# Kernel optimization log

Measured on AMD Instinct MI355X. Metric: run time of the kernel, lower is better.

## Reference

```python
import jax, jax.numpy as jnp
import numpy as np

NUM_SLOTS = 7
DIM = 4096
NUM_HEADS = 8
HEAD_DIM = DIM // NUM_HEADS
LN_EPS = 1e-5


def setup_inputs() -> dict:
    key = jax.random.key(0)
    ks = jax.random.split(key, 9)
    B, N = 8, 2048
    x = jax.random.normal(ks[0], (B, N, DIM), dtype=jnp.float32)
    slots = 1e-4 * jax.random.normal(ks[1], (NUM_SLOTS, DIM), dtype=jnp.float32)
    ln_g = jnp.ones((DIM,), jnp.float32)
    ln_b = jnp.zeros((DIM,), jnp.float32)
    # nn.MultiheadAttention packed in-projection: rows [Wq; Wk; Wv], each (DIM, DIM)
    s = 1.0 / np.sqrt(DIM)
    in_proj_w = jax.random.uniform(ks[2], (3 * DIM, DIM), jnp.float32, -s, s)
    in_proj_b = jnp.zeros((3 * DIM,), jnp.float32)
    out_proj_w = jax.random.uniform(ks[3], (DIM, DIM), jnp.float32, -s, s)
    out_proj_b = jnp.zeros((DIM,), jnp.float32)
    alpha = 0.1 * jax.random.normal(ks[4], (1,), jnp.float32)  # nonzero so gate path is active
    return {"x": x, "slots": slots, "ln_g": ln_g, "ln_b": ln_b,
            "in_proj_w": in_proj_w, "in_proj_b": in_proj_b,
            "out_proj_w": out_proj_w, "out_proj_b": out_proj_b, "alpha": alpha}


def _cmrm(x, slots, ln_g, ln_b, in_proj_w, in_proj_b, out_proj_w, out_proj_b, alpha):
    x32 = x.astype(jnp.float32)
    # pre LayerNorm
    mu = jnp.mean(x32, axis=-1, keepdims=True)
    var = jnp.mean(jnp.square(x32 - mu), axis=-1, keepdims=True)
    xn = (x32 - mu) * jax.lax.rsqrt(var + LN_EPS) * ln_g + ln_b  # (B,N,D)
    slots_c = jnp.clip(slots, -10.0, 10.0)  # (Q,D), Q=7
    Wq, Wk, Wv = jnp.split(in_proj_w, 3, axis=0)
    bq, bk, bv = jnp.split(in_proj_b, 3, axis=0)
    q = slots_c @ Wq.T + bq                      # (Q,D), identical for all batches
    k = xn @ Wk.T + bk                           # (B,N,D)
    v = xn @ Wv.T + bv                           # (B,N,D)
    B, N, _ = x.shape
    qh = q.reshape(NUM_SLOTS, NUM_HEADS, HEAD_DIM)          # (Q,H,hd)
    kh = k.reshape(B, N, NUM_HEADS, HEAD_DIM)
    vh = v.reshape(B, N, NUM_HEADS, HEAD_DIM)
    scale = 1.0 / np.sqrt(HEAD_DIM)
    scores = jnp.einsum('qhd,bnhd->bhqn', qh * scale, kh)   # (B,H,Q,N)
    attn = jax.nn.softmax(scores, axis=-1)
    ctx = jnp.einsum('bhqn,bnhd->bqhd', attn, vh).reshape(B, NUM_SLOTS, DIM)
    slots_out = ctx @ out_proj_w.T + out_proj_b             # (B,Q,D)
    slots_res = slots_c[None] + slots_out                   # residual, ungated slots
    gate = jnp.tanh(alpha)                                  # (1,)
    g = jnp.mean(gate * slots_res, axis=1, keepdims=True)   # (B,1,D)
    x_refined = (x32 + g).astype(x.dtype)
    attn_weights = jnp.mean(attn, axis=1)                   # torch avg over heads -> (B,Q,N)
    return x_refined, attn_weights


def reference(x, slots, ln_g, ln_b, in_proj_w, in_proj_b, out_proj_w, out_proj_b, alpha):
    return _cmrm(x, slots, ln_g, ln_b, in_proj_w, in_proj_b, out_proj_w, out_proj_b, alpha)
```

## Files before the change

kernel.cpp:

```cpp
#include <hip/hip_runtime.h>

typedef __attribute__((ext_vector_type(4))) float f32x4;
typedef __attribute__((ext_vector_type(8))) short short8x;
typedef __attribute__((ext_vector_type(4))) unsigned short u16x4;

#define DIM   4096
#define NB    8
#define NN    2048
#define NROWS (NB*NN)
#define NQ    7
#define NHQ   56
#define SCALE 0.04419417382415922f

#define OFF_MU     0L
#define OFF_RSTD   16384L
#define OFF_Q7     32768L
#define OFF_A      61440L
#define OFF_D0     61504L
#define OFF_S1     61568L
#define OFF_SUMEXP 61632L
#define OFF_CTXM   62528L
#define OFF_GFIN   95296L
#define OFF_YM     128064L
#define OFF_UGBF   390208L
#define OFF_SCT    521280L
#define OFF_BIG    1438784L
#define OFF_PART   (OFF_BIG)
#define OFF_XBF    10000000L

__device__ __forceinline__ unsigned short f2bf(float f) {
  union { float f; unsigned int u; } v; v.f = f;
  return (unsigned short)((v.u + 0x7FFFu + ((v.u >> 16) & 1u)) >> 16);
}
__device__ __forceinline__ unsigned short f2bfr(float f) {
  union { float f; unsigned int u; } v; v.f = f;
  return (unsigned short)((v.u + 0x8000u) >> 16);
}
__device__ __forceinline__ float bf2f(unsigned short u) {
  return __uint_as_float((unsigned)u << 16);
}
__device__ __forceinline__ f32x4 ntl4(const float* p) {
  return __builtin_nontemporal_load((const f32x4*)p);
}
__device__ __forceinline__ void nts4(float* p, f32x4 v) {
  __builtin_nontemporal_store(v, (f32x4*)p);
}
__device__ __forceinline__ float waveSum(float v) {
  #pragma unroll
  for (int m = 1; m < 64; m <<= 1) v += __shfl_xor(v, m);
  return v;
}

__global__ __launch_bounds__(256) void k_pre(const float* __restrict__ ipw,
    const float* __restrict__ ipb, const float* __restrict__ slots,
    float* __restrict__ q7, float* __restrict__ ws) {
  const int bid = blockIdx.x, tid = threadIdx.x;
  const int w = tid >> 6, l = tid & 63;
  if (bid == 0) {
    if (tid < 448) (ws + OFF_SUMEXP)[tid] = 0.f;
    else if (tid < 512) (ws + OFF_S1)[tid - 448] = 0.f;
  } else if (bid <= 8) {
    unsigned* u32 = (unsigned*)(ws + OFF_UGBF);
    const long r = 56 + bid - 1;
    #pragma unroll
    for (int j = 0; j < 8; j++) u32[r*2048 + (long)tid*8 + j] = 0u;
  } else if (bid == 9) {
    if (tid < 64) (ws + OFF_A)[tid] = 0.f;
    else if (tid < 128) (ws + OFF_D0)[tid - 64] = 0.f;
  }
  const int d = bid * 4 + w;
  const float* wr = ipw + (long)d * DIM;
  float acc[7] = {0,0,0,0,0,0,0};
  for (int e4 = l; e4 < 1024; e4 += 64) {
    f32x4 wv = ntl4(wr + e4*4);
    #pragma unroll
    for (int s = 0; s < 7; s++) {
      float4 sv = ((const float4*)(slots + (long)s*DIM))[e4];
      sv.x = fminf(fmaxf(sv.x, -10.f), 10.f); sv.y = fminf(fmaxf(sv.y, -10.f), 10.f);
      sv.z = fminf(fmaxf(sv.z, -10.f), 10.f); sv.w = fminf(fmaxf(sv.w, -10.f), 10.f);
      acc[s] += wv.x*sv.x + wv.y*sv.y + wv.z*sv.z + wv.w*sv.w;
    }
  }
  #pragma unroll
  for (int s = 0; s < 7; s++) acc[s] = waveSum(acc[s]);
  if (l == 0) {
    float bq = ipb[d];
    #pragma unroll
    for (int s = 0; s < 7; s++) q7[(long)s*DIM + d] = acc[s] + bq;
  }
}

__global__ __launch_bounds__(256) void k_uproj(const float* __restrict__ ipw,
    const float* __restrict__ ipb, const float* __restrict__ q7,
    float* __restrict__ upart, float* __restrict__ D0arr) {
  __shared__ float qs[7][32];
  const int bid = blockIdx.x, tid = threadIdx.x;
  const int bx = bid & 3, h = (bid >> 2) & 7, c = bid >> 5;
  if (tid < 224) {
    int s = tid >> 5, hd = tid & 31;
    qs[s][hd] = q7[(long)s*DIM + h*512 + c*32 + hd];
  }
  __syncthreads();
  if (bx == 0 && tid < 64) {
    const int l = tid;
    float bk = (l < 32) ? ipb[DIM + h*512 + c*32 + l] : 0.f;
    #pragma unroll
    for (int s = 0; s < 7; s++) {
      float v = (l < 32) ? qs[s][l]*bk : 0.f;
      v = waveSum(v);
      if (l == 0) atomicAdd(&D0arr[h*7 + s], SCALE * v);
    }
  }
  const int e0 = bx*1024 + tid*4;
  float4 acc[7];
  #pragma unroll
  for (int s = 0; s < 7; s++) { acc[s].x = 0; acc[s].y = 0; acc[s].z = 0; acc[s].w = 0; }
  #pragma unroll 4
  for (int hd = 0; hd < 32; hd++) {
    f32x4 wv = ntl4(ipw + ((long)(DIM + h*512 + c*32 + hd))*DIM + e0);
    #pragma unroll
    for (int s = 0; s < 7; s++) {
      float qv = qs[s][hd];
      acc[s].x += qv*wv.x; acc[s].y += qv*wv.y; acc[s].z += qv*wv.z; acc[s].w += qv*wv.w;
    }
  }
  #pragma unroll
  for (int s = 0; s < 7; s++)
    *(float4*)&upart[(long)((c*8 + h)*7 + s)*DIM + e0] = acc[s];
}

__global__ __launch_bounds__(256) void k_ured(const float* __restrict__ upart,
    const float* __restrict__ lng, const float* __restrict__ lnb,
    unsigned short* __restrict__ ugbf, float* __restrict__ Aarr, float* __restrict__ D0arr) {
  const int bid = blockIdx.x, tid = threadIdx.x;
  const int bx = bid & 15, h = bid >> 4;
  const int e = bx*256 + tid, l = tid & 63;
  float ge = lng[e], be = lnb[e];
  #pragma unroll
  for (int s = 0; s < 7; s++) {
    float u = 0;
    #pragma unroll
    for (int c = 0; c < 16; c++) u += upart[(long)((c*8 + h)*7 + s)*DIM + e];
    u *= SCALE;
    ugbf[(long)(h*7 + s)*DIM + e] = f2bf(u * ge);
    float pa = waveSum(u * ge);
    float pd = waveSum(u * be);
    if (l == 0) {
      atomicAdd(&Aarr[h*7 + s], pa);
      atomicAdd(&D0arr[h*7 + s], pd);
    }
  }
}

__global__ __launch_bounds__(256) void k_scores(const float* __restrict__ x,
    const unsigned short* __restrict__ ugbf, const float* __restrict__ Aarr,
    const float* __restrict__ D0arr, float* __restrict__ mu_o, float* __restrict__ rstd_o,
    float* __restrict__ sct, float* __restrict__ sumexp, unsigned short* __restrict__ xbf) {
  __shared__ __align__(16) unsigned short xs[16][520];
  __shared__ float xch[3][64][16];
  __shared__ float sred[16][2];
  const int tid = threadIdx.x;
  const int w = tid >> 6, l = tid & 63;
  const int lr = l & 15, lk8 = (l >> 4) * 8;
  const int row0 = blockIdx.x * 16;
  const int b = blockIdx.x >> 7;
  const int r = tid >> 4, c = tid & 15;
  const long xrow = (long)(row0 + r) * DIM;
  f32x4 acc0 = {0,0,0,0}, acc1 = {0,0,0,0}, acc2 = {0,0,0,0}, acc3 = {0,0,0,0};
  float sx = 0.f, sxx = 0.f;
  const long b0 = (long)(0*16 + lr)*DIM, b1 = (long)(1*16 + lr)*DIM,
             b2 = (long)(2*16 + lr)*DIM, b3 = (long)(3*16 + lr)*DIM;
  for (int s = 0; s < 8; s++) {
    const int kc0 = s * 512;
    f32x4 v[8];
    #pragma unroll
    for (int j = 0; j < 8; j++)
      v[j] = ntl4(x + xrow + kc0 + j*64 + c*4);
    #pragma unroll
    for (int j = 0; j < 8; j++) {
      sx  += (v[j].x + v[j].y) + (v[j].z + v[j].w);
      sxx += v[j].x*v[j].x + v[j].y*v[j].y + v[j].z*v[j].z + v[j].w*v[j].w;
      u16x4 a;
      a.x = f2bfr(v[j].x); a.y = f2bfr(v[j].y);
      a.z = f2bfr(v[j].z); a.w = f2bfr(v[j].w);
      *(u16x4*)&xs[r][j*64 + c*4] = a;
      *(u16x4*)(xbf + xrow + kc0 + j*64 + c*4) = a;
    }
    __syncthreads();
    const long kw = kc0 + w*128;
    #pragma unroll
    for (int kk = 0; kk < 128; kk += 32) {
      short8x a = *(const short8x*)&xs[lr][w*128 + kk + lk8];
      short8x bb0 = *(const short8x*)(ugbf + b0 + kw + kk + lk8);
      acc0 = __builtin_amdgcn_mfma_f32_16x16x32_bf16(a, bb0, acc0, 0, 0, 0);
      short8x bb1 = *(const short8x*)(ugbf + b1 + kw + kk + lk8);
      acc1 = __builtin_amdgcn_mfma_f32_16x16x32_bf16(a, bb1, acc1, 0, 0, 0);
      short8x bb2 = *(const short8x*)(ugbf + b2 + kw + kk + lk8);
      acc2 = __builtin_amdgcn_mfma_f32_16x16x32_bf16(a, bb2, acc2, 0, 0, 0);
      short8x bb3 = *(const short8x*)(ugbf + b3 + kw + kk + lk8);
      acc3 = __builtin_amdgcn_mfma_f32_16x16x32_bf16(a, bb3, acc3, 0, 0, 0);
    }
    __syncthreads();
  }
  #pragma unroll
  for (int m = 1; m <= 8; m <<= 1) { sx += __shfl_xor(sx, m); sxx += __shfl_xor(sxx, m); }
  if (c == 0) { sred[r][0] = sx; sred[r][1] = sxx; }
  if (w != 0) {
    float* p = xch[w - 1][l];
    #pragma unroll
    for (int i = 0; i < 4; i++) {
      p[i] = acc0[i]; p[4+i] = acc1[i]; p[8+i] = acc2[i]; p[12+i] = acc3[i];
    }
  }
  __syncthreads();
  if (w != 0) return;
  #pragma unroll
  for (int ww = 0; ww < 3; ww++) {
    const float* p = xch[ww][l];
    #pragma unroll
    for (int i = 0; i < 4; i++) {
      acc0[i] += p[i]; acc1[i] += p[4+i]; acc2[i] += p[8+i]; acc3[i] += p[12+i];
    }
  }
  float muv = sred[lr][0] * (1.0f/DIM);
  float var = sred[lr][1] * (1.0f/DIM) - muv*muv;
  float rsv = rsqrtf(var + 1e-5f);
  if (l < 16) { mu_o[row0 + l] = muv; rstd_o[row0 + l] = rsv; }
  float es0 = 0, es1 = 0, es2 = 0, es3 = 0;
  #pragma unroll
  for (int i = 0; i < 4; i++) {
    const int rl = (l >> 4)*4 + i;
    const float mur_ = __shfl(muv, rl);
    const float rs_  = __shfl(rsv, rl);
    {
      int hq = 0*16 + lr; float Ah = Aarr[hq], Dh = D0arr[hq];
      float e = __expf(rs_*(acc0[i] - mur_*Ah) + Dh);
      sct[(long)hq*NROWS + row0 + rl] = e; es0 += e;
    }
    {
      int hq = 1*16 + lr; float Ah = Aarr[hq], Dh = D0arr[hq];
      float e = __expf(rs_*(acc1[i] - mur_*Ah) + Dh);
      sct[(long)hq*NROWS + row0 + rl] = e; es1 += e;
    }
    {
      int hq = 2*16 + lr; float Ah = Aarr[hq], Dh = D0arr[hq];
      float e = __expf(rs_*(acc2[i] - mur_*Ah) + Dh);
      sct[(long)hq*NROWS + row0 + rl] = e; es2 += e;
    }
    if (lr < 8) {
      int hq = 3*16 + lr; float Ah = Aarr[hq], Dh = D0arr[hq];
      float e = __expf(rs_*(acc3[i] - mur_*Ah) + Dh);
      sct[(long)hq*NROWS + row0 + rl] = e; es3 += e;
    }
  }
  es0 += __shfl_xor(es0, 16); es0 += __shfl_xor(es0, 32);
  es1 += __shfl_xor(es1, 16); es1 += __shfl_xor(es1, 32);
  es2 += __shfl_xor(es2, 16); es2 += __shfl_xor(es2, 32);
  es3 += __shfl_xor(es3, 16); es3 += __shfl_xor(es3, 32);
  if (l < 16) {
    atomicAdd(&sumexp[b*NHQ + 0*16 + l], es0);
    atomicAdd(&sumexp[b*NHQ + 1*16 + l], es1);
    atomicAdd(&sumexp[b*NHQ + 2*16 + l], es2);
    if (l < 8) atomicAdd(&sumexp[b*NHQ + 3*16 + l], es3);
  }
}

__global__ __launch_bounds__(256) void k_ypart(const unsigned short* __restrict__ xbf,
    const float* __restrict__ sct, const float* __restrict__ sumexp,
    const float* __restrict__ mu, const float* __restrict__ rstd,
    float* __restrict__ part, float* __restrict__ s1, float* __restrict__ out_attn) {
  __shared__ float rinv[56];
  __shared__ float amr[8][128];
  __shared__ float psm[56][128];
  const int bid = blockIdx.x, tid = threadIdx.x;
  const int b = bid >> 6, ec = (bid >> 4) & 3, nc = bid & 15;
  const int row0 = b*NN + nc*128;
  if (tid < 56) rinv[tid] = 1.0f / sumexp[b*NHQ + tid];
  __syncthreads();
  for (int i = tid; i < 1024; i += 256) {
    const int h = i >> 7, nn = i & 127, row = row0 + nn;
    float amv = 0;
    #pragma unroll
    for (int q = 0; q < 7; q++) {
      float p = sct[(long)(h*7 + q)*NROWS + row] * rinv[h*7 + q];
      amv += p;
      psm[h*7 + q][nn] = p;
    }
    amv *= (1.0f/7.0f);
    amr[h][nn] = amv * rstd[row];
  }
  __syncthreads();
  if (ec == 0) {
    for (int i = tid; i < 896; i += 256) {
      const int q = i / 128, nn = i % 128;
      float s = 0;
      #pragma unroll
      for (int h = 0; h < 8; h++) s += psm[h*7 + q][nn];
      out_attn[((long)(b*NQ + q))*NN + nc*128 + nn] = s * 0.125f;
    }
    {
      const int h = tid >> 5, sl = tid & 31;
      float v = 0;
      #pragma unroll
      for (int nn = sl; nn < 128; nn += 32) v += amr[h][nn] * mu[row0 + nn];
      #pragma unroll
      for (int m = 1; m < 32; m <<= 1) v += __shfl_xor(v, m);
      if (sl == 0) atomicAdd(&s1[b*8 + h], v);
    }
  }
  const int e = ec*1024 + tid*4;
  float ax[8], ay[8], az[8], aw[8];
  #pragma unroll
  for (int h = 0; h < 8; h++) { ax[h]=0; ay[h]=0; az[h]=0; aw[h]=0; }
  const unsigned short* xp = xbf + (long)row0*DIM + e;
  #pragma unroll 2
  for (int nn = 0; nn < 128; nn++) {
    const u16x4 xv = *(const u16x4*)(xp + (long)nn*DIM);
    const float xx = bf2f(xv.x), xy = bf2f(xv.y), xz = bf2f(xv.z), xw = bf2f(xv.w);
    #pragma unroll
    for (int h = 0; h < 8; h++) {
      float a = amr[h][nn];
      ax[h] += a*xx; ay[h] += a*xy; az[h] += a*xz; aw[h] += a*xw;
    }
  }
  #pragma unroll
  for (int h = 0; h < 8; h++) {
    float4 o; o.x = ax[h]; o.y = ay[h]; o.z = az[h]; o.w = aw[h];
    *(float4*)&part[((long)(nc*64 + b*8 + h))*DIM + e] = o;
  }
}

__global__ __launch_bounds__(256) void k_yred(const float* __restrict__ part,
    const float* __restrict__ s1, const float* __restrict__ lng, const float* __restrict__ lnb,
    float* __restrict__ ym) {
  const long i4 = (long)blockIdx.x*256 + threadIdx.x;
  const float4* p4 = (const float4*)part;
  float4 s = p4[i4];
  #pragma unroll
  for (int nc = 1; nc < 16; nc++) {
    float4 v = p4[(long)nc*65536 + i4];
    s.x += v.x; s.y += v.y; s.z += v.z; s.w += v.w;
  }
  const int bh = (int)(i4 >> 10), e4 = (int)(i4 & 1023);
  float sv = s1[bh];
  float4 g = ((const float4*)lng)[e4], bb = ((const float4*)lnb)[e4];
  float4 o;
  o.x = g.x*(s.x - sv) + bb.x; o.y = g.y*(s.y - sv) + bb.y;
  o.z = g.z*(s.z - sv) + bb.z; o.w = g.w*(s.w - sv) + bb.w;
  ((float4*)ym)[i4] = o;
}

__global__ __launch_bounds__(256) void k_ctxm(const float* __restrict__ ipw,
    const float* __restrict__ ipb, const float* __restrict__ ym, float* __restrict__ ctxm) {
  const int w = threadIdx.x >> 6, l = threadIdx.x & 63;
  const int d = blockIdx.x*4 + w;
  const int h = d >> 9;
  const float* wr = ipw + ((long)(2*DIM + d))*DIM;
  float acc[8] = {0,0,0,0,0,0,0,0};
  for (int e4 = l; e4 < 1024; e4 += 64) {
    f32x4 wv = ntl4(wr + e4*4);
    #pragma unroll
    for (int b = 0; b < 8; b++) {
      float4 y = ((const float4*)(ym + (long)(b*8 + h)*DIM))[e4];
      acc[b] += wv.x*y.x + wv.y*y.y + wv.z*y.z + wv.w*y.w;
    }
  }
  #pragma unroll
  for (int b = 0; b < 8; b++) acc[b] = waveSum(acc[b]);
  if (l == 0) {
    float bias = ipb[2*DIM + d];
    #pragma unroll
    for (int b = 0; b < 8; b++) ctxm[(long)b*DIM + d] = acc[b] + bias;
  }
}

__global__ __launch_bounds__(256) void k_gvec(const float* __restrict__ opw,
    const float* __restrict__ opb, const float* __restrict__ ctxm, const float* __restrict__ slots,
    const float* __restrict__ alpha, float* __restrict__ gfin) {
  const int w = threadIdx.x >> 6, l = threadIdx.x & 63;
  const int d = blockIdx.x*4 + w;
  const float* wr = opw + (long)d*DIM;
  float acc[8] = {0,0,0,0,0,0,0,0};
  for (int e4 = l; e4 < 1024; e4 += 64) {
    f32x4 wv = ntl4(wr + e4*4);
    #pragma unroll
    for (int b = 0; b < 8; b++) {
      float4 c = ((const float4*)(ctxm + (long)b*DIM))[e4];
      acc[b] += wv.x*c.x + wv.y*c.y + wv.z*c.z + wv.w*c.w;
    }
  }
  #pragma unroll
  for (int b = 0; b < 8; b++) acc[b] = waveSum(acc[b]);
  if (l == 0) {
    float smv = 0;
    #pragma unroll
    for (int q = 0; q < 7; q++)
      smv += fminf(fmaxf(slots[(long)q*DIM + d], -10.f), 10.f);
    smv *= (1.0f/7.0f);
    float t = tanhf(alpha[0]);
    float base = smv + opb[d];
    #pragma unroll
    for (int b = 0; b < 8; b++) gfin[(long)b*DIM + d] = t * (base + acc[b]);
  }
}

__global__ __launch_bounds__(256) void k_refine(const unsigned short* __restrict__ xbf,
    const float* __restrict__ gfin, float* __restrict__ out) {
  const float4* g4 = (const float4*)gfin;
  const long total = (long)NROWS * 1024;
  for (long i4 = (long)blockIdx.x*256 + threadIdx.x; i4 < total; i4 += (long)gridDim.x*256) {
    const long b = i4 >> 21;
    const int e4 = (int)(i4 & 1023);
    const u16x4 xv = *(const u16x4*)(xbf + i4*4);
    const float4 gv = g4[b*1024 + e4];
    f32x4 o;
    o.x = bf2f(xv.x) + gv.x; o.y = bf2f(xv.y) + gv.y;
    o.z = bf2f(xv.z) + gv.z; o.w = bf2f(xv.w) + gv.w;
    nts4(out + i4*4, o);
  }
}

extern "C" void kernel_launch(void* const* d_in, const int* in_sizes, int n_in,
                              void* d_out, int out_size, void* d_ws, size_t ws_size,
                              hipStream_t stream) {
  const float* x     = (const float*)d_in[0];
  const float* slots = (const float*)d_in[1];
  const float* lng   = (const float*)d_in[2];
  const float* lnb   = (const float*)d_in[3];
  const float* ipw   = (const float*)d_in[4];
  const float* ipb   = (const float*)d_in[5];
  const float* opw   = (const float*)d_in[6];
  const float* opb   = (const float*)d_in[7];
  const float* alpha = (const float*)d_in[8];
  float* out = (float*)d_out;
  float* ws  = (float*)d_ws;

  float* mu     = ws + OFF_MU;
  float* rstd   = ws + OFF_RSTD;
  float* q7     = ws + OFF_Q7;
  float* Aarr   = ws + OFF_A;
  float* D0arr  = ws + OFF_D0;
  float* s1     = ws + OFF_S1;
  float* sumexp = ws + OFF_SUMEXP;
  float* ctxm   = ws + OFF_CTXM;
  float* gfin   = ws + OFF_GFIN;
  float* ym     = ws + OFF_YM;
  unsigned short* ugbf = (unsigned short*)(ws + OFF_UGBF);
  float* sct    = ws + OFF_SCT;
  float* upart  = ws + OFF_BIG;
  float* part   = ws + OFF_PART;
  unsigned short* xbf = (unsigned short*)(ws + OFF_XBF);
  float* out_attn = out + (long)NROWS * DIM;

  hipLaunchKernelGGL(k_pre,    dim3(1024), dim3(256), 0, stream, ipw, ipb, slots, q7, ws);
  hipLaunchKernelGGL(k_uproj,  dim3(512),  dim3(256), 0, stream, ipw, ipb, q7, upart, D0arr);
  hipLaunchKernelGGL(k_ured,   dim3(128),  dim3(256), 0, stream, upart, lng, lnb, ugbf, Aarr, D0arr);
  hipLaunchKernelGGL(k_scores, dim3(1024), dim3(256), 0, stream, x, ugbf, Aarr, D0arr, mu, rstd, sct, sumexp, xbf);
  hipLaunchKernelGGL(k_ypart,  dim3(512),  dim3(256), 0, stream, xbf, sct, sumexp, mu, rstd, part, s1, out_attn);
  hipLaunchKernelGGL(k_yred,   dim3(256),  dim3(256), 0, stream, part, s1, lng, lnb, ym);
  hipLaunchKernelGGL(k_ctxm,   dim3(1024), dim3(256), 0, stream, ipw, ipb, ym, ctxm);
  hipLaunchKernelGGL(k_gvec,   dim3(1024), dim3(256), 0, stream, opw, opb, ctxm, slots, alpha, gfin);
  hipLaunchKernelGGL(k_refine, dim3(8192), dim3(256), 0, stream, xbf, gfin, out);
}
```

Baseline: 348.1 us.

## Double-buffer x tiles in k_scores to overlap global loads with MFMA

The k_scores loop now uses two LDS buffers and prefetches the next 512-column chunk of x into registers while the current chunk's MFMAs run. It then converts the prefetched data to bf16 and writes it to the other buffer. This halves the barriers per iteration and hides global load latency behind compute. Each thread also handles 8 contiguous elements (16-byte bf16 stores) instead of 4, widening the LDS and xbf stores. The cost is doubled LDS for xs and higher register pressure from the prefetch registers, which could reduce occupancy.

New measurement: 388.1 us. +11.5%, slower.

```diff
diff --git a/kernel.cpp b/kernel.cpp
--- a/kernel.cpp
+++ b/kernel.cpp
@@ -156,7 +156,7 @@
     const unsigned short* __restrict__ ugbf, const float* __restrict__ Aarr,
     const float* __restrict__ D0arr, float* __restrict__ mu_o, float* __restrict__ rstd_o,
     float* __restrict__ sct, float* __restrict__ sumexp, unsigned short* __restrict__ xbf) {
-  __shared__ __align__(16) unsigned short xs[16][520];
+  __shared__ __align__(16) unsigned short xs[2][16][520];
   __shared__ float xch[3][64][16];
   __shared__ float sred[16][2];
   const int tid = threadIdx.x;
@@ -170,27 +170,44 @@
   float sx = 0.f, sxx = 0.f;
   const long b0 = (long)(0*16 + lr)*DIM, b1 = (long)(1*16 + lr)*DIM,
              b2 = (long)(2*16 + lr)*DIM, b3 = (long)(3*16 + lr)*DIM;
+  {
+    f32x4 v[8];
+    #pragma unroll
+    for (int j = 0; j < 4; j++) {
+      v[2*j]   = ntl4(x + xrow + j*128 + c*8);
+      v[2*j+1] = ntl4(x + xrow + j*128 + c*8 + 4);
+    }
+    #pragma unroll
+    for (int j = 0; j < 4; j++) {
+      f32x4 p = v[2*j], q = v[2*j+1];
+      sx  += (p.x + p.y) + (p.z + p.w) + (q.x + q.y) + (q.z + q.w);
+      sxx += p.x*p.x + p.y*p.y + p.z*p.z + p.w*p.w
+           + q.x*q.x + q.y*q.y + q.z*q.z + q.w*q.w;
+      short8x o;
+      o[0] = (short)f2bfr(p.x); o[1] = (short)f2bfr(p.y);
+      o[2] = (short)f2bfr(p.z); o[3] = (short)f2bfr(p.w);
+      o[4] = (short)f2bfr(q.x); o[5] = (short)f2bfr(q.y);
+      o[6] = (short)f2bfr(q.z); o[7] = (short)f2bfr(q.w);
+      *(short8x*)&xs[0][r][j*128 + c*8] = o;
+      *(short8x*)(xbf + xrow + j*128 + c*8) = o;
+    }
+  }
+  __syncthreads();
   for (int s = 0; s < 8; s++) {
-    const int kc0 = s * 512;
-    f32x4 v[8];
-    #pragma unroll
-    for (int j = 0; j < 8; j++)
-      v[j] = ntl4(x + xrow + kc0 + j*64 + c*4);
-    #pragma unroll
-    for (int j = 0; j < 8; j++) {
-      sx  += (v[j].x + v[j].y) + (v[j].z + v[j].w);
-      sxx += v[j].x*v[j].x + v[j].y*v[j].y + v[j].z*v[j].z + v[j].w*v[j].w;
-      u16x4 a;
-      a.x = f2bfr(v[j].x); a.y = f2bfr(v[j].y);
-      a.z = f2bfr(v[j].z); a.w = f2bfr(v[j].w);
-      *(u16x4*)&xs[r][j*64 + c*4] = a;
-      *(u16x4*)(xbf + xrow + kc0 + j*64 + c*4) = a;
-    }
-    __syncthreads();
-    const long kw = kc0 + w*128;
+    f32x4 vn[8];
+    if (s < 7) {
+      const long kn = xrow + (s + 1)*512;
+      #pragma unroll
+      for (int j = 0; j < 4; j++) {
+        vn[2*j]   = ntl4(x + kn + j*128 + c*8);
+        vn[2*j+1] = ntl4(x + kn + j*128 + c*8 + 4);
+      }
+    }
+    const int kw = s*512 + w*128;
+    const unsigned short* xsrow = &xs[s & 1][lr][w*128 + lk8];
     #pragma unroll
     for (int kk = 0; kk < 128; kk += 32) {
-      short8x a = *(const short8x*)&xs[lr][w*128 + kk + lk8];
+      short8x a = *(const short8x*)(xsrow + kk);
       short8x bb0 = *(const short8x*)(ugbf + b0 + kw + kk + lk8);
       acc0 = __builtin_amdgcn_mfma_f32_16x16x32_bf16(a, bb0, acc0, 0, 0, 0);
       short8x bb1 = *(const short8x*)(ugbf + b1 + kw + kk + lk8);
@@ -199,6 +216,24 @@
       acc2 = __builtin_amdgcn_mfma_f32_16x16x32_bf16(a, bb2, acc2, 0, 0, 0);
       short8x bb3 = *(const short8x*)(ugbf + b3 + kw + kk + lk8);
       acc3 = __builtin_amdgcn_mfma_f32_16x16x32_bf16(a, bb3, acc3, 0, 0, 0);
+    }
+    if (s < 7) {
+      const long kn = xrow + (s + 1)*512;
+      const int buf = (s + 1) & 1;
+      #pragma unroll
+      for (int j = 0; j < 4; j++) {
+        f32x4 p = vn[2*j], q = vn[2*j+1];
+        sx  += (p.x + p.y) + (p.z + p.w) + (q.x + q.y) + (q.z + q.w);
+        sxx += p.x*p.x + p.y*p.y + p.z*p.z + p.w*p.w
+             + q.x*q.x + q.y*q.y + q.z*q.z + q.w*q.w;
+        short8x o;
+        o[0] = (short)f2bfr(p.x); o[1] = (short)f2bfr(p.y);
+        o[2] = (short)f2bfr(p.z); o[3] = (short)f2bfr(p.w);
+        o[4] = (short)f2bfr(q.x); o[5] = (short)f2bfr(q.y);
+        o[6] = (short)f2bfr(q.z); o[7] = (short)f2bfr(q.w);
+        *(short8x*)&xs[buf][r][j*128 + c*8] = o;
+        *(short8x*)(xbf + kn + j*128 + c*8) = o;
+      }
     }
     __syncthreads();
   }
```
